# Kernel optimization log

Measured on AMD Instinct MI355X. Metric: run time of the kernel, lower is better.

## Reference

```python
import jax, jax.numpy as jnp
import numpy as np
from jax import lax

# Module config (mirrors init_kwargs)
N, CIN, COUT, H, W = 16, 512, 512, 64, 64
KS = 3          # conv kernel_size
FACTOR = 2
GAIN = 1.0
LRMUL = 1.0
FIR_1D = np.array([1.0, 3.0, 3.0, 1.0], dtype=np.float32)

# upfirdn pad amounts as in the torch code
FIRN = 4
P = FIRN - FACTOR + (KS - 1)      # = 4
PAD0 = (P + 1) // 2               # = 2
PAD1 = P // 2                     # = 2
W_LRMUL = GAIN / np.sqrt(CIN * COUT * KS * KS)  # he_std * lrmul (use_wscale)
B_LRMUL = LRMUL
SQRT2 = np.float32(np.sqrt(2.0))


def setup_inputs() -> dict:
    key = jax.random.key(0)
    kx, kw, kb = jax.random.split(key, 3)
    x = jax.random.normal(kx, (N, CIN, H, W), dtype=jnp.float32)
    # weight init: randn * init_std, init_std = 1/lrmul = 1.0 under use_wscale
    weight = jax.random.normal(kw, (COUT, CIN, KS, KS), dtype=jnp.float32)
    bias = jax.random.normal(kb, (COUT,), dtype=jnp.float32) * 0.1
    kf = np.outer(FIR_1D, FIR_1D)
    kf = kf / kf.sum() * GAIN
    fir = jnp.asarray(kf, dtype=jnp.float32)  # [4,4], non-trainable
    return {"x": x, "weight": weight, "bias": bias, "fir": fir}


def _blur_and_resize(x, fir):
    # x: [N, C, H, W]; FIR blur via depthwise trick: fold C into batch.
    n, c, h, w = x.shape
    y = x.reshape(n * c, 1, h, w)
    y = jnp.pad(y, ((0, 0), (0, 0), (PAD0, PAD1), (PAD0, PAD1)))
    # valid conv with 4x4 FIR -> [n*c, 1, h+1, w+1]
    y = lax.conv_general_dilated(
        y, fir[None, None, :, :], window_strides=(1, 1), padding="VALID",
        dimension_numbers=("NCHW", "OIHW", "NCHW"))
    # F.interpolate(mode='nearest') from (h+1, w+1) back to (h, w):
    # torch nearest uses src = floor(dst * in/out) == (dst*(h+1))//h
    ri = (jnp.arange(h) * (h + 1)) // h
    ci = (jnp.arange(w) * (w + 1)) // w
    y = y[:, :, ri, :][:, :, :, ci]
    return y.reshape(n, c, h, w)


def reference(x, weight, bias, fir):
    y = _blur_and_resize(x, fir)
    # strided conv: stride=factor, padding=ks//2 (SAME-ish), cross-correlation
    out = lax.conv_general_dilated(
        y, weight * W_LRMUL, window_strides=(FACTOR, FACTOR),
        padding=[(KS // 2, KS // 2), (KS // 2, KS // 2)],
        dimension_numbers=("NCHW", "OIHW", "NCHW"))
    out = out + (bias * B_LRMUL)[None, :, None, None]
    out = jnp.where(out >= 0, out, 0.2 * out) * SQRT2  # leaky_relu(0.2) * sqrt(2)
    return out
```

## Files before the change

### kernel.cpp

```cpp
#include <hip/hip_runtime.h>
#include <hip/hip_bf16.h>
#include <stdint.h>

#define N_IMG 16
#define C_IN  512
#define C_OUT 512
#define H_IN  64
#define W_IN  64
#define OH    32
#define OW    32
#define PIX   (N_IMG*OH*OW)

#define YPH 65
#define YPW 33

#define W2_ELEMS (9*C_OUT*C_IN)
#define W2_BYTES (W2_ELEMS*2)

#define BM 128
#define BN 256
#define BK 64
#define NKT 72
#define ATILE_B (BM*BK*2)
#define BTILE_B (BN*BK*2)
#define BUF_B   (ATILE_B+BTILE_B)
#define LDS_TOTAL (3*BUF_B)

typedef __attribute__((ext_vector_type(8))) __bf16 bf16x8;
typedef __attribute__((ext_vector_type(4))) float  f32x4;

__device__ inline void gload_lds16(const void* g, void* l) {
  __builtin_amdgcn_global_load_lds(
      (const __attribute__((address_space(1))) void*)g,
      (__attribute__((address_space(3))) void*)l, 16, 0, 0);
}

#define WAIT_VM(N) asm volatile("s_waitcnt vmcnt(" #N ")" ::: "memory")
#define WAIT_LGKM0 asm volatile("s_waitcnt lgkmcnt(0)" ::: "memory")
__device__ inline void barrier_raw() {
  asm volatile("" ::: "memory");
  __builtin_amdgcn_s_barrier();
  asm volatile("" ::: "memory");
}

struct TagMain  { static constexpr bool stg = true;  static constexpr int vn = 6;  };
struct TagTail0 { static constexpr bool stg = false; static constexpr int vn = 0;  };
struct TagTail1 { static constexpr bool stg = false; static constexpr int vn = -1; };

__global__ __launch_bounds__(256) void prep_w_kernel(const float* __restrict__ w,
                                                     __hip_bfloat16* __restrict__ w2) {
  int id = blockIdx.x * 256 + threadIdx.x;
  const float* p = w + (size_t)id * 9;
  float v[9];
#pragma unroll
  for (int t = 0; t < 9; ++t) v[t] = p[t] * (1.0f/1536.0f);
#pragma unroll
  for (int t = 0; t < 9; ++t)
    w2[(size_t)t*(C_OUT*C_IN) + id] = __float2bfloat16(v[t]);
}

__global__ __launch_bounds__(256) void blur_kernel(const float* __restrict__ x,
                                                   __hip_bfloat16* __restrict__ yt) {
  __shared__ float obuf[2][32][65];
  const int tid = threadIdx.x;
  const int c   = tid >> 3;
  const int p8  = tid & 7;
  const int w8  = p8 * 8;
  const int r0  = blockIdx.x * 8;
  const int cib = blockIdx.y;
  const int n   = blockIdx.z;
  const float* xc = x + ((size_t)(n*C_IN + cib*32 + c) * H_IN) * W_IN + w8;

  {
    const uint4 z4 = {0u, 0u, 0u, 0u};
    if (tid < 16) {
      int hh  = r0 + (tid >> 1);
      int par = tid & 1;
      size_t slot = (((size_t)n*YPH + hh + 1)*2 + par)*YPW;
      uint4* p = (uint4*)(yt + slot*C_IN + cib*32);
      p[0]=z4; p[1]=z4; p[2]=z4; p[3]=z4;
    }
    if (blockIdx.x == 0 && tid < 66) {
      int par = tid / 33;
      int cc  = tid - par*33;
      size_t slot = ((size_t)n*YPH*2 + par)*YPW + cc;
      uint4* p = (uint4*)(yt + slot*C_IN + cib*32);
      p[0]=z4; p[1]=z4; p[2]=z4; p[3]=z4;
    }
  }

  const int rp_oc  = tid & 3;
  const int rp_p   = tid >> 2;
  const int rp_par = rp_p & 1;
  const int rp_ch  = rp_p >> 1;

  float cur[8], nxt[8];
  float h1[8], h2[8], h3[8];
#pragma unroll
  for (int j = 0; j < 8; ++j) { h1[j] = 0.f; h2[j] = 0.f; h3[j] = 0.f; }

  auto load_row = [&](int r, float* dst) {
    if (r >= 0 && r < H_IN) {
      const float4 a = *(const float4*)(xc + (size_t)r * W_IN);
      const float4 b = *(const float4*)(xc + (size_t)r * W_IN + 4);
      dst[0]=a.x; dst[1]=a.y; dst[2]=a.z; dst[3]=a.w;
      dst[4]=b.x; dst[5]=b.y; dst[6]=b.z; dst[7]=b.w;
    } else {
#pragma unroll
      for (int j = 0; j < 8; ++j) dst[j] = 0.f;
    }
  };

  load_row(r0 - 2, cur);
  for (int ri = 0; ri < 11; ++ri) {
    const int r = r0 - 2 + ri;
    if (ri < 10) load_row(r + 1, nxt);

    float l2 = __shfl_up(cur[6], 1);
    float l1 = __shfl_up(cur[7], 1);
    float rr = __shfl_down(cur[0], 1);
    if (p8 == 0) { l2 = 0.f; l1 = 0.f; }
    if (p8 == 7) { rr = 0.f; }
    float hc[8];
    hc[0] = l2 + 3.f*(l1 + cur[0]) + cur[1];
    hc[1] = l1 + 3.f*(cur[0] + cur[1]) + cur[2];
#pragma unroll
    for (int j = 2; j < 7; ++j) hc[j] = cur[j-2] + 3.f*(cur[j-1] + cur[j]) + cur[j+1];
    hc[7] = cur[5] + 3.f*(cur[6] + cur[7]) + rr;

    if (ri >= 3) {
      const int h = r - 1;
      const int b = ri & 1;
#pragma unroll
      for (int j = 0; j < 8; ++j)
        obuf[b][c][w8 + j] = (h3[j] + 3.f*(h2[j] + h1[j]) + hc[j]) * (1.0f/64.0f);
      __syncthreads();
      alignas(16) __hip_bfloat16 t16[8];
#pragma unroll
      for (int j = 0; j < 8; ++j)
        t16[j] = __float2bfloat16(obuf[b][rp_oc*8 + j][rp_p]);
      size_t slot = ((size_t)(n*YPH + h + 1)*2 + rp_par)*YPW + rp_ch + 1;
      *(uint4*)(yt + slot*C_IN + cib*32 + rp_oc*8) = *(uint4*)t16;
    }

#pragma unroll
    for (int j = 0; j < 8; ++j) {
      h3[j] = h2[j]; h2[j] = h1[j]; h1[j] = hc[j]; cur[j] = nxt[j];
    }
  }
}

__global__ __launch_bounds__(512, 2) void conv_kernel(const __hip_bfloat16* __restrict__ w2,
                            const __hip_bfloat16* __restrict__ yt,
                            const float* __restrict__ bias,
                            float* __restrict__ out) {
  extern __shared__ char lds[];
  const int tid   = threadIdx.x;
  const int lane  = tid & 63;
  const int wv    = tid >> 6;
  const int wvb64 = wv * 64;
  const int wm    = wv & 1;
  const int wn    = wv >> 1;
  const int cob0  = blockIdx.y * BM;
  const int pixb  = blockIdx.x * BN;
  const int quad  = lane >> 4;

  size_t aoff[2];
#pragma unroll
  for (int i = 0; i < 2; ++i) {
    int s = i*512 + tid, r = s >> 3, p = s & 7, g = p ^ (r & 7);
    aoff[i] = (size_t)(cob0 + r)*C_IN + g*8;
  }
  int bn65[4], boh2[4], bow_[4], bseg8[4];
#pragma unroll
  for (int i = 0; i < 4; ++i) {
    int s = i*512 + tid, r = s >> 3, p = s & 7, g = p ^ (r & 7);
    int gp = pixb + r;
    bn65[i]  = (gp >> 10) * YPH;
    boh2[i]  = ((gp >> 5) & 31) * 2;
    bow_[i]  = gp & 31;
    bseg8[i] = g*8;
  }

  int aRdOff[4][2], bRdOff[4][2];
#pragma unroll
  for (int f = 0; f < 4; ++f) {
    int ra = wm*64 + f*16 + (lane & 15);
    int rb = wn*64 + f*16 + (lane & 15);
#pragma unroll
    for (int kk = 0; kk < 2; ++kk) {
      aRdOff[f][kk] = ra*128 + (((kk*4 + quad) ^ (ra & 7)) * 16);
      bRdOff[f][kk] = rb*128 + (((kk*4 + quad) ^ (rb & 7)) * 16);
    }
  }

  struct BP { int kh, par, d, cib; };
  auto bparams = [&](int kt) {
    const int t  = kt >> 3;
    const int kh = (t * 11) >> 5;
    const int kw = t - kh*3;
    BP r; r.kh = kh; r.par = (kw == 1) ? 0 : 1; r.d = (kw == 0) ? 0 : 1;
    r.cib = (kt & 7) << 6;
    return r;
  };
  auto stageA = [&](int kt, int b) {
    const int t = kt >> 3;
    const __hip_bfloat16* wt = w2 + (size_t)t*(C_OUT*C_IN) + ((kt & 7) << 6);
    char* da = lds + b*BUF_B;
    gload_lds16(wt + aoff[0], da + (size_t)(      wvb64)*16);
    gload_lds16(wt + aoff[1], da + (size_t)(512 + wvb64)*16);
  };
  auto stageB01 = [&](BP bp, int b) {
    char* db = lds + b*BUF_B + ATILE_B;
    size_t s0 = ((size_t)(bn65[0] + boh2[0] + bp.kh)*2 + bp.par)*YPW + bow_[0] + bp.d;
    gload_lds16(yt + s0*C_IN + bseg8[0] + bp.cib, db + (size_t)(      wvb64)*16);
    size_t s1 = ((size_t)(bn65[1] + boh2[1] + bp.kh)*2 + bp.par)*YPW + bow_[1] + bp.d;
    gload_lds16(yt + s1*C_IN + bseg8[1] + bp.cib, db + (size_t)(512 + wvb64)*16);
  };
  auto stageB23 = [&](BP bp, int b) {
    char* db = lds + b*BUF_B + ATILE_B;
    size_t s2 = ((size_t)(bn65[2] + boh2[2] + bp.kh)*2 + bp.par)*YPW + bow_[2] + bp.d;
    gload_lds16(yt + s2*C_IN + bseg8[2] + bp.cib, db + (size_t)(1024 + wvb64)*16);
    size_t s3 = ((size_t)(bn65[3] + boh2[3] + bp.kh)*2 + bp.par)*YPW + bow_[3] + bp.d;
    gload_lds16(yt + s3*C_IN + bseg8[3] + bp.cib, db + (size_t)(1536 + wvb64)*16);
  };

  f32x4 acc[4][4];
  const f32x4 zero = {0.f, 0.f, 0.f, 0.f};
#pragma unroll
  for (int mi = 0; mi < 4; ++mi)
#pragma unroll
    for (int ni = 0; ni < 4; ++ni) acc[mi][ni] = zero;

  {
    BP b0 = bparams(0);
    stageA(0, 0); stageB01(b0, 0); stageB23(b0, 0);
    BP b1 = bparams(1);
    stageA(1, 1); stageB01(b1, 1); stageB23(b1, 1);
    WAIT_VM(6);
    barrier_raw();
  }

  auto body = [&](int k, int cb, int sb, auto tag) {
    using T = decltype(tag);
    const char* Ab = lds + cb*BUF_B;
    const char* Bb = Ab + ATILE_B;
    BP bp{};
    if constexpr (T::stg) bp = bparams(k + 2);

    bf16x8 af[4][2], b0[2], b1[2];
#pragma unroll
    for (int mi = 0; mi < 4; ++mi)
#pragma unroll
      for (int kk = 0; kk < 2; ++kk)
        af[mi][kk] = *(const bf16x8*)(Ab + aRdOff[mi][kk]);
#pragma unroll
    for (int kk = 0; kk < 2; ++kk) {
      b0[kk] = *(const bf16x8*)(Bb + bRdOff[0][kk]);
      b1[kk] = *(const bf16x8*)(Bb + bRdOff[1][kk]);
    }
    if constexpr (T::stg) { stageA(k + 2, sb); stageB01(bp, sb); }
    barrier_raw();
    WAIT_LGKM0;
    __builtin_amdgcn_sched_barrier(0);
    __builtin_amdgcn_s_setprio(1);
#pragma unroll
    for (int kk = 0; kk < 2; ++kk)
#pragma unroll
      for (int mi = 0; mi < 4; ++mi) {
        acc[mi][0] = __builtin_amdgcn_mfma_f32_16x16x32_bf16(af[mi][kk], b0[kk], acc[mi][0], 0, 0, 0);
        acc[mi][1] = __builtin_amdgcn_mfma_f32_16x16x32_bf16(af[mi][kk], b1[kk], acc[mi][1], 0, 0, 0);
      }
    __builtin_amdgcn_s_setprio(0);
    barrier_raw();

    bf16x8 b2[2], b3[2];
#pragma unroll
    for (int kk = 0; kk < 2; ++kk) {
      b2[kk] = *(const bf16x8*)(Bb + bRdOff[2][kk]);
      b3[kk] = *(const bf16x8*)(Bb + bRdOff[3][kk]);
    }
    if constexpr (T::stg) stageB23(bp, sb);
    if constexpr (T::vn == 6) WAIT_VM(6);
    else if constexpr (T::vn == 0) WAIT_VM(0);
    barrier_raw();
    WAIT_LGKM0;
    __builtin_amdgcn_sched_barrier(0);
    __builtin_amdgcn_s_setprio(1);
#pragma unroll
    for (int kk = 0; kk < 2; ++kk)
#pragma unroll
      for (int mi = 0; mi < 4; ++mi) {
        acc[mi][2] = __builtin_amdgcn_mfma_f32_16x16x32_bf16(af[mi][kk], b2[kk], acc[mi][2], 0, 0, 0);
        acc[mi][3] = __builtin_amdgcn_mfma_f32_16x16x32_bf16(af[mi][kk], b3[kk], acc[mi][3], 0, 0, 0);
      }
    __builtin_amdgcn_s_setprio(0);
    barrier_raw();
  };

  int cb = 0, sb = 2;
  for (int k = 0; k < NKT - 2; ++k) {
    body(k, cb, sb, TagMain{});
    cb = (cb == 2) ? 0 : cb + 1;
    sb = (sb == 2) ? 0 : sb + 1;
  }
  body(NKT - 2, cb, sb, TagTail0{});
  cb = (cb == 2) ? 0 : cb + 1;
  body(NKT - 1, cb, 0, TagTail1{});

#pragma unroll
  for (int mi = 0; mi < 4; ++mi) {
#pragma unroll
    for (int reg = 0; reg < 4; ++reg) {
      int co = cob0 + wm*64 + mi*16 + quad*4 + reg;
      float bv = bias[co];
#pragma unroll
      for (int ni = 0; ni < 4; ++ni) {
        int gp  = pixb + wn*64 + ni*16 + (lane & 15);
        int n   = gp >> 10;
        int ohw = gp & 1023;
        float v = acc[mi][ni][reg] + bv;
        v = (v >= 0.f ? v : 0.2f*v) * 1.41421356f;
        out[(((size_t)n*C_OUT + co) << 10) + ohw] = v;
      }
    }
  }
}

extern "C" void kernel_launch(void* const* d_in, const int* in_sizes, int n_in,
                              void* d_out, int out_size, void* d_ws, size_t ws_size,
                              hipStream_t stream) {
  const float* x    = (const float*)d_in[0];
  const float* w    = (const float*)d_in[1];
  const float* bias = (const float*)d_in[2];
  float* out = (float*)d_out;
  __hip_bfloat16* w2 = (__hip_bfloat16*)d_ws;
  __hip_bfloat16* yt = (__hip_bfloat16*)((char*)d_ws + W2_BYTES);

  static bool attr_set = false;
  if (!attr_set) {
    hipFuncSetAttribute(reinterpret_cast<const void*>(conv_kernel),
                        hipFuncAttributeMaxDynamicSharedMemorySize, LDS_TOTAL);
    attr_set = true;
  }

  prep_w_kernel<<<(C_OUT*C_IN)/256, 256, 0, stream>>>(w, w2);
  blur_kernel<<<dim3(8, 16, 16), 256, 0, stream>>>(x, yt);
  conv_kernel<<<dim3(PIX/BN, C_OUT/BM), 512, LDS_TOTAL, stream>>>(w2, yt, bias, out);
}
```

Baseline: 306.7 us.

## Collapse two-phase ping-pong main loop into single-barrier phase per K-tile

Replaces the two-half body (B01 then B23, each with barriers, lgkmcnt waits and sched_barriers) with one phase per K-tile. All A and B fragments are read up front, the whole next tile is staged at once, then all 32 MFMAs are issued, with a single barrier per iteration. The goal is to cut barrier and synchronisation overhead from four barriers per tile down to one. In exchange it gives up the interleaving of LDS reads and MFMA across halves and holds more fragment registers live at once.

After: 302.0 us, median of 2. Within noise of the previous version (-1.5%).

```diff
diff --git a/kernel.cpp b/kernel.cpp
--- a/kernel.cpp
+++ b/kernel.cpp
@@ -36,7 +36,6 @@
 }
 
 #define WAIT_VM(N) asm volatile("s_waitcnt vmcnt(" #N ")" ::: "memory")
-#define WAIT_LGKM0 asm volatile("s_waitcnt lgkmcnt(0)" ::: "memory")
 __device__ inline void barrier_raw() {
   asm volatile("" ::: "memory");
   __builtin_amdgcn_s_barrier();
@@ -203,26 +202,19 @@
     r.cib = (kt & 7) << 6;
     return r;
   };
-  auto stageA = [&](int kt, int b) {
+  auto stageTile = [&](int kt, int b) {
     const int t = kt >> 3;
     const __hip_bfloat16* wt = w2 + (size_t)t*(C_OUT*C_IN) + ((kt & 7) << 6);
     char* da = lds + b*BUF_B;
     gload_lds16(wt + aoff[0], da + (size_t)(      wvb64)*16);
     gload_lds16(wt + aoff[1], da + (size_t)(512 + wvb64)*16);
-  };
-  auto stageB01 = [&](BP bp, int b) {
-    char* db = lds + b*BUF_B + ATILE_B;
-    size_t s0 = ((size_t)(bn65[0] + boh2[0] + bp.kh)*2 + bp.par)*YPW + bow_[0] + bp.d;
-    gload_lds16(yt + s0*C_IN + bseg8[0] + bp.cib, db + (size_t)(      wvb64)*16);
-    size_t s1 = ((size_t)(bn65[1] + boh2[1] + bp.kh)*2 + bp.par)*YPW + bow_[1] + bp.d;
-    gload_lds16(yt + s1*C_IN + bseg8[1] + bp.cib, db + (size_t)(512 + wvb64)*16);
-  };
-  auto stageB23 = [&](BP bp, int b) {
-    char* db = lds + b*BUF_B + ATILE_B;
-    size_t s2 = ((size_t)(bn65[2] + boh2[2] + bp.kh)*2 + bp.par)*YPW + bow_[2] + bp.d;
-    gload_lds16(yt + s2*C_IN + bseg8[2] + bp.cib, db + (size_t)(1024 + wvb64)*16);
-    size_t s3 = ((size_t)(bn65[3] + boh2[3] + bp.kh)*2 + bp.par)*YPW + bow_[3] + bp.d;
-    gload_lds16(yt + s3*C_IN + bseg8[3] + bp.cib, db + (size_t)(1536 + wvb64)*16);
+    BP bp = bparams(kt);
+    char* db = da + ATILE_B;
+#pragma unroll
+    for (int i = 0; i < 4; ++i) {
+      size_t s = ((size_t)(bn65[i] + boh2[i] + bp.kh)*2 + bp.par)*YPW + bow_[i] + bp.d;
+      gload_lds16(yt + s*C_IN + bseg8[i] + bp.cib, db + (size_t)(i*512 + wvb64)*16);
+    }
   };
 
   f32x4 acc[4][4];
@@ -232,69 +224,42 @@
 #pragma unroll
     for (int ni = 0; ni < 4; ++ni) acc[mi][ni] = zero;
 
-  {
-    BP b0 = bparams(0);
-    stageA(0, 0); stageB01(b0, 0); stageB23(b0, 0);
-    BP b1 = bparams(1);
-    stageA(1, 1); stageB01(b1, 1); stageB23(b1, 1);
-    WAIT_VM(6);
-    barrier_raw();
-  }
+  stageTile(0, 0);
+  stageTile(1, 1);
+  WAIT_VM(6);
+  barrier_raw();
 
   auto body = [&](int k, int cb, int sb, auto tag) {
     using T = decltype(tag);
     const char* Ab = lds + cb*BUF_B;
     const char* Bb = Ab + ATILE_B;
-    BP bp{};
-    if constexpr (T::stg) bp = bparams(k + 2);
-
-    bf16x8 af[4][2], b0[2], b1[2];
+
+    bf16x8 af[4][2], bfv[4][2];
 #pragma unroll
     for (int mi = 0; mi < 4; ++mi)
 #pragma unroll
       for (int kk = 0; kk < 2; ++kk)
         af[mi][kk] = *(const bf16x8*)(Ab + aRdOff[mi][kk]);
 #pragma unroll
-    for (int kk = 0; kk < 2; ++kk) {
-      b0[kk] = *(const bf16x8*)(Bb + bRdOff[0][kk]);
-      b1[kk] = *(const bf16x8*)(Bb + bRdOff[1][kk]);
-    }
-    if constexpr (T::stg) { stageA(k + 2, sb); stageB01(bp, sb); }
-    barrier_raw();
-    WAIT_LGKM0;
-    __builtin_amdgcn_sched_barrier(0);
+    for (int ni = 0; ni < 4; ++ni)
+#pragma unroll
+      for (int kk = 0; kk < 2; ++kk)
+        bfv[ni][kk] = *(const bf16x8*)(Bb + bRdOff[ni][kk]);
+
+    if constexpr (T::stg) stageTile(k + 2, sb);
+
     __builtin_amdgcn_s_setprio(1);
 #pragma unroll
     for (int kk = 0; kk < 2; ++kk)
 #pragma unroll
-      for (int mi = 0; mi < 4; ++mi) {
-        acc[mi][0] = __builtin_amdgcn_mfma_f32_16x16x32_bf16(af[mi][kk], b0[kk], acc[mi][0], 0, 0, 0);
-        acc[mi][1] = __builtin_amdgcn_mfma_f32_16x16x32_bf16(af[mi][kk], b1[kk], acc[mi][1], 0, 0, 0);
-      }
+      for (int mi = 0; mi < 4; ++mi)
+#pragma unroll
+        for (int ni = 0; ni < 4; ++ni)
+          acc[mi][ni] = __builtin_amdgcn_mfma_f32_16x16x32_bf16(af[mi][kk], bfv[ni][kk], acc[mi][ni], 0, 0, 0);
     __builtin_amdgcn_s_setprio(0);
-    barrier_raw();
-
-    bf16x8 b2[2], b3[2];
-#pragma unroll
-    for (int kk = 0; kk < 2; ++kk) {
-      b2[kk] = *(const bf16x8*)(Bb + bRdOff[2][kk]);
-      b3[kk] = *(const bf16x8*)(Bb + bRdOff[3][kk]);
-    }
-    if constexpr (T::stg) stageB23(bp, sb);
+
     if constexpr (T::vn == 6) WAIT_VM(6);
     else if constexpr (T::vn == 0) WAIT_VM(0);
-    barrier_raw();
-    WAIT_LGKM0;
-    __builtin_amdgcn_sched_barrier(0);
-    __builtin_amdgcn_s_setprio(1);
-#pragma unroll
-    for (int kk = 0; kk < 2; ++kk)
-#pragma unroll
-      for (int mi = 0; mi < 4; ++mi) {
-        acc[mi][2] = __builtin_amdgcn_mfma_f32_16x16x32_bf16(af[mi][kk], b2[kk], acc[mi][2], 0, 0, 0);
-        acc[mi][3] = __builtin_amdgcn_mfma_f32_16x16x32_bf16(af[mi][kk], b3[kk], acc[mi][3], 0, 0, 0);
-      }
-    __builtin_amdgcn_s_setprio(0);
     barrier_raw();
   };
 
```
